# Kernel optimization log

Measured on AMD Instinct MI355X. Metric: run time of the kernel, lower is better.

## Reference

```python
import jax, jax.numpy as jnp
import numpy as np

B, S, E, H = 4, 2048, 1024, 16
D = E // H  # head_size = 64

def setup_inputs() -> dict:
    key = jax.random.key(0)
    ks = jax.random.split(key, 10)
    s_e = E ** -0.5
    s_4e = (4 * E) ** -0.5
    inp = {
        "x": jax.random.normal(ks[0], (B, S, E), dtype=jnp.float32),
        # per-head Q/K/V weights, stacked: [H, E, D], no bias
        "Wq": jax.random.normal(ks[1], (H, E, D), dtype=jnp.float32) * s_e,
        "Wk": jax.random.normal(ks[2], (H, E, D), dtype=jnp.float32) * s_e,
        "Wv": jax.random.normal(ks[3], (H, E, D), dtype=jnp.float32) * s_e,
        "Wo": jax.random.normal(ks[4], (E, E), dtype=jnp.float32) * s_e,
        "bo": jax.random.normal(ks[5], (E,), dtype=jnp.float32) * 0.01,
        "W1": jax.random.normal(ks[6], (E, 4 * E), dtype=jnp.float32) * s_e,
        "b1": jax.random.normal(ks[7], (4 * E,), dtype=jnp.float32) * 0.01,
        "W2": jax.random.normal(ks[8], (4 * E, E), dtype=jnp.float32) * s_4e,
        "b2": jax.random.normal(ks[9], (E,), dtype=jnp.float32) * 0.01,
    }
    return inp

def reference(x, Wq, Wk, Wv, Wo, bo, W1, b1, W2, b2):
    b, s, e = x.shape
    # NOTE: original scales by embedding_size**-0.5 (Size of x), not head_size
    scale = e ** -0.5
    q = jnp.einsum("bse,hed->bhsd", x, Wq)
    k = jnp.einsum("bse,hed->bhsd", x, Wk)
    v = jnp.einsum("bse,hed->bhsd", x, Wv)
    scores = jnp.einsum("bhsd,bhtd->bhst", q, k) * scale
    causal = jnp.tril(jnp.ones((s, s), dtype=bool))
    scores = jnp.where(causal, scores, -jnp.inf)
    weights = jax.nn.softmax(scores, axis=-1)
    attn = jnp.einsum("bhst,bhtd->bhsd", weights, v)  # [B,H,S,D]
    # concat heads along last dim: [B,S,H*D]
    attn = attn.transpose(0, 2, 1, 3).reshape(b, s, e)
    y = attn @ Wo + bo
    x = x + y  # residual (no LayerNorm applied in original forward)
    h = jax.nn.relu(x @ W1 + b1)
    ffn = h @ W2 + b2
    return x + ffn
```

## Files before the change

kernel.cpp:

```cpp
#include <hip/hip_runtime.h>
#include <stdint.h>

#define B_ 4
#define S_ 2048
#define E_ 1024
#define H_ 16
#define D_ 64

typedef unsigned short u16;
typedef u16 u16x8 __attribute__((ext_vector_type(8)));
typedef __bf16 bf16x8 __attribute__((ext_vector_type(8)));
typedef float f32x4 __attribute__((ext_vector_type(4)));

__device__ __forceinline__ float bf2f(u16 x) {
  unsigned int v = ((unsigned int)x) << 16;
  return __builtin_bit_cast(float, v);
}
__device__ __forceinline__ u16 f2bf(float f) {
  unsigned int u = __builtin_bit_cast(unsigned int, f);
  unsigned int r = (u + 0x7fffu + ((u >> 16) & 1u)) >> 16;
  return (u16)r;
}

__device__ __forceinline__ void gl2lds16(const u16* g, u16* l) {
  __builtin_amdgcn_global_load_lds(
      (const __attribute__((address_space(1))) void*)g,
      (__attribute__((address_space(3))) void*)l, 16, 0, 0);
}

__global__ __launch_bounds__(256) void cast_bf16_k(const float* __restrict__ src,
                                                   u16* __restrict__ dst, long n) {
  long i = ((long)blockIdx.x * 256 + threadIdx.x) * 8;
  if (i + 8 <= n) {
    f32x4 a = *(const f32x4*)(src + i), b = *(const f32x4*)(src + i + 4);
    u16x8 o;
#pragma unroll
    for (int j = 0; j < 4; j++) { o[j] = f2bf(a[j]); o[j + 4] = f2bf(b[j]); }
    *(u16x8*)(dst + i) = o;
  }
}

__global__ __launch_bounds__(256) void castT_k(const float* __restrict__ src,
                                               u16* __restrict__ dst, int R, int C) {
  long bofs = (long)blockIdx.z * R * C;
  src += bofs; dst += bofs;
  __shared__ u16 t[32][33];
  int c0 = blockIdx.x * 32, r0 = blockIdx.y * 32;
  int lc = threadIdx.x & 31, lr8 = threadIdx.x >> 5;
#pragma unroll
  for (int i = 0; i < 4; i++) {
    int lr = lr8 + i * 8;
    t[lr][lc] = f2bf(src[(long)(r0 + lr) * C + c0 + lc]);
  }
  __syncthreads();
#pragma unroll
  for (int i = 0; i < 4; i++) {
    int lr = lr8 + i * 8;
    dst[(long)(c0 + lr) * R + r0 + lc] = t[lc][lr];
  }
}

__global__ __launch_bounds__(256) void vT_k(const u16* __restrict__ QKV,
                                            u16* __restrict__ VTg) {
  int bh = blockIdx.z, d0 = blockIdx.y * 32, t0 = blockIdx.x * 32;
  int b = bh >> 4, h = bh & 15;
  __shared__ u16 t[32][33];
  int lc = threadIdx.x & 31, lr8 = threadIdx.x >> 5;
#pragma unroll
  for (int i = 0; i < 4; i++) {
    int lr = lr8 + i * 8;
    t[lr][lc] = QKV[(long)(b * S_ + t0 + lr) * 3072 + 2048 + h * 64 + d0 + lc];
  }
  __syncthreads();
#pragma unroll
  for (int i = 0; i < 4; i++) {
    int lr = lr8 + i * 8;
    VTg[((long)bh * 64 + d0 + lr) * S_ + t0 + lc] = t[lc][lr];
  }
}

template <bool AF32, bool CF32>
__global__ __launch_bounds__(256) void gemm128(const void* __restrict__ Av,
                                               const u16* __restrict__ BT,
                                               void* __restrict__ Cv,
                                               const float* __restrict__ bias,
                                               const float* __restrict__ resid,
                                               int M, int N, int K, int relu,
                                               u16* __restrict__ Cbf) {
  __shared__ u16 As[128 * 32];
  __shared__ u16 Bs[128 * 32];
  const int tid = threadIdx.x;
  const int wave = tid >> 6, lane = tid & 63;
  const int m0 = blockIdx.y * 128, n0 = blockIdx.x * 128;
  const int wm = wave >> 1, wn = wave & 1;
  const int fr = lane & 15, quad = lane >> 4;

  f32x4 acc[4][4] = {};

  const int srow = wave * 32 + (lane >> 2);
  const int skcol = (lane & 3) * 8;

  for (int k0 = 0; k0 < K; k0 += 32) {
    __syncthreads();
    if (AF32) {
      const float* Ap = (const float*)Av + (long)(m0 + (tid >> 1)) * K + k0 + (tid & 1) * 16;
      f32x4 f0 = *(const f32x4*)Ap, f1 = *(const f32x4*)(Ap + 4);
      f32x4 f2 = *(const f32x4*)(Ap + 8), f3 = *(const f32x4*)(Ap + 12);
      u16x8 p0, p1;
#pragma unroll
      for (int j = 0; j < 4; j++) {
        p0[j] = f2bf(f0[j]); p0[j + 4] = f2bf(f1[j]);
        p1[j] = f2bf(f2[j]); p1[j + 4] = f2bf(f3[j]);
      }
      *(u16x8*)&As[(tid >> 1) * 32 + (tid & 1) * 16] = p0;
      *(u16x8*)&As[(tid >> 1) * 32 + (tid & 1) * 16 + 8] = p1;
    } else {
      const u16* Ag = (const u16*)Av + (long)(m0 + srow) * K + k0 + skcol;
      gl2lds16(Ag, &As[(wave * 32) * 32]);
      gl2lds16(Ag + 16 * (long)K, &As[(wave * 32 + 16) * 32]);
    }
    {
      const u16* Bg = BT + (long)(n0 + srow) * K + k0 + skcol;
      gl2lds16(Bg, &Bs[(wave * 32) * 32]);
      gl2lds16(Bg + 16 * (long)K, &Bs[(wave * 32 + 16) * 32]);
    }
    __syncthreads();

    bf16x8 af[4], bfr[4];
#pragma unroll
    for (int mi = 0; mi < 4; mi++)
      af[mi] = __builtin_bit_cast(bf16x8, *(const u16x8*)&As[(wm * 64 + mi * 16 + fr) * 32 + quad * 8]);
#pragma unroll
    for (int ni = 0; ni < 4; ni++)
      bfr[ni] = __builtin_bit_cast(bf16x8, *(const u16x8*)&Bs[(wn * 64 + ni * 16 + fr) * 32 + quad * 8]);
#pragma unroll
    for (int mi = 0; mi < 4; mi++)
#pragma unroll
      for (int ni = 0; ni < 4; ni++)
        acc[mi][ni] = __builtin_amdgcn_mfma_f32_16x16x32_bf16(af[mi], bfr[ni], acc[mi][ni], 0, 0, 0);
  }

#pragma unroll
  for (int mi = 0; mi < 4; mi++)
#pragma unroll
    for (int ni = 0; ni < 4; ni++)
#pragma unroll
      for (int r = 0; r < 4; r++) {
        int gm = m0 + wm * 64 + mi * 16 + quad * 4 + r;
        int gn = n0 + wn * 64 + ni * 16 + fr;
        float v = acc[mi][ni][r];
        if (bias) v += bias[gn];
        if (resid) v += resid[(long)gm * N + gn];
        if (relu) v = fmaxf(v, 0.f);
        if (CF32) ((float*)Cv)[(long)gm * N + gn] = v;
        else      ((u16*)Cv)[(long)gm * N + gn] = f2bf(v);
        if (Cbf) Cbf[(long)gm * N + gn] = f2bf(v);
      }
}

__device__ __forceinline__ bf16x8 ldfrag32(const u16* base, int r, int quad) {
  int u = (r * 32 + quad * 8) ^ (((r >> 3) & 1) << 4);
  return __builtin_bit_cast(bf16x8, *(const u16x8*)(base + u));
}

template <bool CF32>
__global__ __launch_bounds__(512) void gemm2ph(const u16* __restrict__ A,
                                               const u16* __restrict__ BT,
                                               void* __restrict__ Cv,
                                               const float* __restrict__ bias,
                                               const float* __restrict__ resid,
                                               int M, int N, int K, int relu,
                                               u16* __restrict__ Cbf) {
  (void)M;
  constexpr int BM = 256, BN = 128, BK = 32;
  constexpr int AU = BM * BK;
  constexpr int BU = BN * BK;
  constexpr int BUF = AU + BU;

  __shared__ u16 sm[2 * BUF];
  const int tid = threadIdx.x;
  const int wave = tid >> 6, lane = tid & 63;
  const int wm = wave >> 1, wn = wave & 1;
  const int fr = lane & 15, quad = lane >> 4;

  const int nbx = gridDim.x;
  const int nwg = nbx * (int)gridDim.y;
  const int wgid = blockIdx.y * nbx + blockIdx.x;
  const int qq = nwg >> 3, rr = nwg & 7;
  const int xcd = wgid & 7, loc = wgid >> 3;
  const int sw = (xcd < rr ? xcd * (qq + 1) : rr * (qq + 1) + (xcd - rr) * qq) + loc;
  const int n0 = (sw % nbx) * BN;
  const int m0 = (sw / nbx) * BM;

  const int NT = K / BK;

  f32x4 acc[4][4] = {};

  const int sc_ = (tid & 3) * 8;
  const int sr_ = tid >> 2;
  const int wbase = wave << 9;

  const int rA = wm * 64 + fr;
  const int rB = wn * 64 + fr;

  {
    u16* buf = sm;
#pragma unroll
    for (int h = 0; h < 2; h++) {
      int r = h * 128 + sr_;
      int c = sc_ ^ (((r >> 3) & 1) << 4);
      gl2lds16(A + (size_t)(m0 + r) * K + c, buf + h * 4096 + wbase);
    }
    {
      int c = sc_ ^ (((sr_ >> 3) & 1) << 4);
      gl2lds16(BT + (size_t)(n0 + sr_) * K + c, buf + AU + wbase);
    }
  }
  asm volatile("s_waitcnt vmcnt(0)" ::: "memory");
  __builtin_amdgcn_s_barrier();

  for (int t = 0; t < NT; ++t) {
    u16* cb = sm + (t & 1) * BUF;
    u16* nb = sm + ((t + 1) & 1) * BUF;

    if (t + 1 < NT) {
      const int k0 = (t + 1) * BK;
#pragma unroll
      for (int h = 0; h < 2; h++) {
        int r = h * 128 + sr_;
        int c = sc_ ^ (((r >> 3) & 1) << 4);
        gl2lds16(A + (size_t)(m0 + r) * K + k0 + c, nb + h * 4096 + wbase);
      }
      {
        int c = sc_ ^ (((sr_ >> 3) & 1) << 4);
        gl2lds16(BT + (size_t)(n0 + sr_) * K + k0 + c, nb + AU + wbase);
      }
    }

    bf16x8 aF[4], bF[4];
#pragma unroll
    for (int mi = 0; mi < 4; ++mi) aF[mi] = ldfrag32(cb, rA + mi * 16, quad);
#pragma unroll
    for (int ni = 0; ni < 4; ++ni) bF[ni] = ldfrag32(cb + AU, rB + ni * 16, quad);

    asm volatile("s_waitcnt lgkmcnt(0)" ::: "memory");
    __builtin_amdgcn_sched_barrier(0);
    __builtin_amdgcn_s_setprio(1);
#pragma unroll
    for (int mi = 0; mi < 4; ++mi)
#pragma unroll
      for (int ni = 0; ni < 4; ++ni)
        acc[mi][ni] = __builtin_amdgcn_mfma_f32_16x16x32_bf16(aF[mi], bF[ni], acc[mi][ni], 0, 0, 0);
    __builtin_amdgcn_s_setprio(0);

    asm volatile("s_waitcnt vmcnt(0)" ::: "memory");
    __builtin_amdgcn_s_barrier();
  }

#pragma unroll
  for (int mi = 0; mi < 4; ++mi)
#pragma unroll
    for (int ni = 0; ni < 4; ++ni)
#pragma unroll
      for (int r = 0; r < 4; ++r) {
        int gm = m0 + wm * 64 + mi * 16 + quad * 4 + r;
        int gn = n0 + wn * 64 + ni * 16 + fr;
        float v = acc[mi][ni][r];
        if (bias) v += bias[gn];
        if (resid) v += resid[(long)gm * N + gn];
        if (relu) v = fmaxf(v, 0.f);
        if (CF32) ((float*)Cv)[(long)gm * N + gn] = v;
        else      ((u16*)Cv)[(long)gm * N + gn] = f2bf(v);
        if (Cbf) Cbf[(long)gm * N + gn] = f2bf(v);
      }
}

__global__ __launch_bounds__(256) void attn_mfma3(const u16* __restrict__ QKV,
                                                  const u16* __restrict__ VTg,
                                                  u16* __restrict__ attn) {
  int p = blockIdx.x, h = blockIdx.y, b = blockIdx.z;
  int tid = threadIdx.x;
  int wq = tid >> 6, lane = tid & 63;
  int fr = lane & 15, quad = lane >> 4;
  int kf = quad * 8;

  __shared__ u16 Qs[64][72];
  __shared__ u16 Ks[64][72];
  __shared__ u16 Vt[64][72];
  __shared__ u16 Ps[4][16][72];

  const u16* base = QKV + (long)b * S_ * 3072;
  const u16* vbase = VTg + (long)(b * 16 + h) * 64 * S_;
  int st = tid >> 2;
  int sd = (tid & 3) * 16;

  for (int ti = 0; ti < 2; ti++) {
    int qt = ti ? (31 - p) : p;

    {
      const u16* qr = base + (long)(qt * 64 + st) * 3072 + h * 64 + sd;
      u16x8 a = *(const u16x8*)qr, d = *(const u16x8*)(qr + 8);
      u16x8 oa, od;
#pragma unroll
      for (int j = 0; j < 8; j++) {
        oa[j] = f2bf(bf2f(a[j]) * 0.03125f);
        od[j] = f2bf(bf2f(d[j]) * 0.03125f);
      }
      *(u16x8*)&Qs[st][sd] = oa;
      *(u16x8*)&Qs[st][sd + 8] = od;
    }
    __syncthreads();
    bf16x8 qf0 = __builtin_bit_cast(bf16x8, *(const u16x8*)&Qs[wq * 16 + fr][kf]);
    bf16x8 qf1 = __builtin_bit_cast(bf16x8, *(const u16x8*)&Qs[wq * 16 + fr][32 + kf]);

    f32x4 acc[4] = {};
    float l[4] = {0.f, 0.f, 0.f, 0.f};

    for (int c = 0; c <= qt; c++) {
      int t0 = c * 64;
      __syncthreads();
      {
        const u16* kr = base + (long)(t0 + st) * 3072 + 1024 + h * 64 + sd;
        u16x8 k0 = *(const u16x8*)kr, k1 = *(const u16x8*)(kr + 8);
        const u16* vr = vbase + (long)st * S_ + t0 + sd;
        u16x8 v0 = *(const u16x8*)vr, v1 = *(const u16x8*)(vr + 8);
        *(u16x8*)&Ks[st][sd] = k0;
        *(u16x8*)&Ks[st][sd + 8] = k1;
        *(u16x8*)&Vt[st][sd] = v0;
        *(u16x8*)&Vt[st][sd + 8] = v1;
      }
      __syncthreads();

      f32x4 sc[4] = {};
#pragma unroll
      for (int nt = 0; nt < 4; nt++) {
        bf16x8 b0 = __builtin_bit_cast(bf16x8, *(const u16x8*)&Ks[nt * 16 + fr][kf]);
        bf16x8 b1 = __builtin_bit_cast(bf16x8, *(const u16x8*)&Ks[nt * 16 + fr][32 + kf]);
        sc[nt] = __builtin_amdgcn_mfma_f32_16x16x32_bf16(qf0, b0, sc[nt], 0, 0, 0);
        sc[nt] = __builtin_amdgcn_mfma_f32_16x16x32_bf16(qf1, b1, sc[nt], 0, 0, 0);
      }

      if (c == qt) {
        int qloc = wq * 16 + quad * 4;
#pragma unroll
        for (int nt = 0; nt < 4; nt++)
#pragma unroll
          for (int r = 0; r < 4; r++)
            if (nt * 16 + fr > qloc + r) sc[nt][r] = -1e30f;
      }

#pragma unroll
      for (int nt = 0; nt < 4; nt++)
#pragma unroll
        for (int r = 0; r < 4; r++) {
          float pv = __expf(sc[nt][r]);
          sc[nt][r] = pv;
          l[r] += pv;
        }

#pragma unroll
      for (int nt = 0; nt < 4; nt++)
#pragma unroll
        for (int r = 0; r < 4; r++)
          Ps[wq][quad * 4 + r][nt * 16 + fr] = f2bf(sc[nt][r]);

      bf16x8 pa0 = __builtin_bit_cast(bf16x8, *(const u16x8*)&Ps[wq][fr][kf]);
      bf16x8 pa1 = __builtin_bit_cast(bf16x8, *(const u16x8*)&Ps[wq][fr][32 + kf]);
#pragma unroll
      for (int nt = 0; nt < 4; nt++) {
        bf16x8 vb0 = __builtin_bit_cast(bf16x8, *(const u16x8*)&Vt[nt * 16 + fr][kf]);
        bf16x8 vb1 = __builtin_bit_cast(bf16x8, *(const u16x8*)&Vt[nt * 16 + fr][32 + kf]);
        acc[nt] = __builtin_amdgcn_mfma_f32_16x16x32_bf16(pa0, vb0, acc[nt], 0, 0, 0);
        acc[nt] = __builtin_amdgcn_mfma_f32_16x16x32_bf16(pa1, vb1, acc[nt], 0, 0, 0);
      }
    }

#pragma unroll
    for (int r = 0; r < 4; r++)
#pragma unroll
      for (int off = 1; off < 16; off <<= 1) l[r] += __shfl_xor(l[r], off);

    long row = (long)b * S_ + qt * 64 + wq * 16 + quad * 4;
#pragma unroll
    for (int nt = 0; nt < 4; nt++)
#pragma unroll
      for (int r = 0; r < 4; r++)
        attn[(row + r) * 1024 + h * 64 + nt * 16 + fr] = f2bf(acc[nt][r] / l[r]);
  }
}

extern "C" void kernel_launch(void* const* d_in, const int* in_sizes, int n_in,
                              void* d_out, int out_size, void* d_ws, size_t ws_size,
                              hipStream_t stream) {
  (void)in_sizes; (void)n_in; (void)out_size;
  const float* x  = (const float*)d_in[0];
  const float* Wq = (const float*)d_in[1];
  const float* Wk = (const float*)d_in[2];
  const float* Wv = (const float*)d_in[3];
  const float* Wo = (const float*)d_in[4];
  const float* bo = (const float*)d_in[5];
  const float* W1 = (const float*)d_in[6];
  const float* b1 = (const float*)d_in[7];
  const float* W2 = (const float*)d_in[8];
  const float* b2 = (const float*)d_in[9];
  float* out = (float*)d_out;

  char* ws = (char*)d_ws;
  u16*   QKV  = (u16*)(ws);
  u16*   attn = (u16*)(ws + 50331648);
  u16*   hbuf = (u16*)(ws);
  float* x1   = (float*)(ws + 67108864);
  u16*   VTg  = (u16*)(ws + 67108864);
  u16*   xb   = (u16*)(ws + 83886080);
  u16*   WT   = (u16*)(ws + 100663296);
  u16*   WoT  = (u16*)(ws + 106954752);
  u16*   W1T  = (u16*)(ws + 109051904);
  u16*   W2T  = (u16*)(ws + 117440512);
  u16*   x1b  = (u16*)(ws + 125829120);
  bool bigws = ws_size >= (size_t)142606336;

  cast_bf16_k<<<4096, 256, 0, stream>>>(x, xb, (long)8192 * 1024);
  castT_k<<<dim3(2, 32, 16), 256, 0, stream>>>(Wq, WT, 1024, 64);
  castT_k<<<dim3(2, 32, 16), 256, 0, stream>>>(Wk, WT + 1048576, 1024, 64);
  castT_k<<<dim3(2, 32, 16), 256, 0, stream>>>(Wv, WT + 2097152, 1024, 64);
  castT_k<<<dim3(32, 32, 1), 256, 0, stream>>>(Wo, WoT, 1024, 1024);
  castT_k<<<dim3(128, 32, 1), 256, 0, stream>>>(W1, W1T, 1024, 4096);
  castT_k<<<dim3(32, 128, 1), 256, 0, stream>>>(W2, W2T, 4096, 1024);

  gemm2ph<false><<<dim3(24, 32), 512, 0, stream>>>(xb, WT, QKV, nullptr, nullptr, 8192, 3072, 1024, 0, nullptr);
  vT_k<<<dim3(64, 2, 64), 256, 0, stream>>>(QKV, VTg);
  attn_mfma3<<<dim3(16, H_, B_), 256, 0, stream>>>(QKV, VTg, attn);
  gemm2ph<true><<<dim3(8, 32), 512, 0, stream>>>(attn, WoT, x1, bo, x, 8192, 1024, 1024, 0, bigws ? x1b : nullptr);
  if (bigws)
    gemm2ph<false><<<dim3(32, 32), 512, 0, stream>>>(x1b, W1T, hbuf, b1, nullptr, 8192, 4096, 1024, 1, nullptr);
  else
    gemm128<true, false><<<dim3(32, 64), 256, 0, stream>>>(x1, W1T, hbuf, b1, nullptr, 8192, 4096, 1024, 1, nullptr);
  gemm2ph<true><<<dim3(8, 32), 512, 0, stream>>>(hbuf, W2T, out, b2, x1, 8192, 1024, 4096, 0, nullptr);
}
```

Baseline: 561.1 us.

## Triple-buffer LDS in GEMM kernel to prefetch two K-tiles ahead

Replaces the double-buffered GEMM main loop with a three-stage LDS ring that issues global-to-LDS loads two K iterations ahead. Each wait uses vmcnt(3) so only the older tile's loads must finish, which lets one tile's loads stay in flight across the MFMA block. The aim is to hide global memory latency behind compute in all four GEMMs. In exchange, LDS use rises from 48KB to 72KB per block, which could lower occupancy.

```diff
diff --git a/kernel.cpp b/kernel.cpp
--- a/kernel.cpp
+++ b/kernel.cpp
@@ -163,21 +163,35 @@
   return __builtin_bit_cast(bf16x8, *(const u16x8*)(base + u));
 }
 
+__device__ __forceinline__ void stage_tile(const u16* __restrict__ A,
+                                           const u16* __restrict__ BT, int K,
+                                           int m0, int n0, int k0,
+                                           u16* __restrict__ buf,
+                                           int sr_, int sc_, int wbase) {
+#pragma unroll
+  for (int h = 0; h < 2; h++) {
+    int r = h * 128 + sr_;
+    int c = sc_ ^ (((r >> 3) & 1) << 4);
+    gl2lds16(A + (size_t)(m0 + r) * K + k0 + c, buf + h * 4096 + wbase);
+  }
+  int c = sc_ ^ (((sr_ >> 3) & 1) << 4);
+  gl2lds16(BT + (size_t)(n0 + sr_) * K + k0 + c, buf + 8192 + wbase);
+}
+
 template <bool CF32>
-__global__ __launch_bounds__(512) void gemm2ph(const u16* __restrict__ A,
-                                               const u16* __restrict__ BT,
-                                               void* __restrict__ Cv,
-                                               const float* __restrict__ bias,
-                                               const float* __restrict__ resid,
-                                               int M, int N, int K, int relu,
-                                               u16* __restrict__ Cbf) {
+__global__ __launch_bounds__(512) void gemm3b(const u16* __restrict__ A,
+                                              const u16* __restrict__ BT,
+                                              void* __restrict__ Cv,
+                                              const float* __restrict__ bias,
+                                              const float* __restrict__ resid,
+                                              int M, int N, int K, int relu,
+                                              u16* __restrict__ Cbf) {
   (void)M;
   constexpr int BM = 256, BN = 128, BK = 32;
   constexpr int AU = BM * BK;
-  constexpr int BU = BN * BK;
-  constexpr int BUF = AU + BU;
-
-  __shared__ u16 sm[2 * BUF];
+  constexpr int BUF = AU + BN * BK;
+
+  __shared__ u16 sm[3 * BUF];
   const int tid = threadIdx.x;
   const int wave = tid >> 6, lane = tid & 63;
   const int wm = wave >> 1, wn = wave & 1;
@@ -203,38 +217,22 @@
   const int rA = wm * 64 + fr;
   const int rB = wn * 64 + fr;
 
-  {
-    u16* buf = sm;
-#pragma unroll
-    for (int h = 0; h < 2; h++) {
-      int r = h * 128 + sr_;
-      int c = sc_ ^ (((r >> 3) & 1) << 4);
-      gl2lds16(A + (size_t)(m0 + r) * K + c, buf + h * 4096 + wbase);
-    }
-    {
-      int c = sc_ ^ (((sr_ >> 3) & 1) << 4);
-      gl2lds16(BT + (size_t)(n0 + sr_) * K + c, buf + AU + wbase);
-    }
-  }
-  asm volatile("s_waitcnt vmcnt(0)" ::: "memory");
+  stage_tile(A, BT, K, m0, n0, 0, sm, sr_, sc_, wbase);
+  if (NT > 1) {
+    stage_tile(A, BT, K, m0, n0, BK, sm + BUF, sr_, sc_, wbase);
+    asm volatile("s_waitcnt vmcnt(3)" ::: "memory");
+  } else {
+    asm volatile("s_waitcnt vmcnt(0)" ::: "memory");
+  }
   __builtin_amdgcn_s_barrier();
 
+  int cur = 0;
   for (int t = 0; t < NT; ++t) {
-    u16* cb = sm + (t & 1) * BUF;
-    u16* nb = sm + ((t + 1) & 1) * BUF;
-
-    if (t + 1 < NT) {
-      const int k0 = (t + 1) * BK;
-#pragma unroll
-      for (int h = 0; h < 2; h++) {
-        int r = h * 128 + sr_;
-        int c = sc_ ^ (((r >> 3) & 1) << 4);
-        gl2lds16(A + (size_t)(m0 + r) * K + k0 + c, nb + h * 4096 + wbase);
-      }
-      {
-        int c = sc_ ^ (((sr_ >> 3) & 1) << 4);
-        gl2lds16(BT + (size_t)(n0 + sr_) * K + k0 + c, nb + AU + wbase);
-      }
+    u16* cb = sm + cur * BUF;
+
+    if (t + 2 < NT) {
+      int s2 = cur + 2; if (s2 >= 3) s2 -= 3;
+      stage_tile(A, BT, K, m0, n0, (t + 2) * BK, sm + s2 * BUF, sr_, sc_, wbase);
     }
 
     bf16x8 aF[4], bF[4];
@@ -253,8 +251,10 @@
         acc[mi][ni] = __builtin_amdgcn_mfma_f32_16x16x32_bf16(aF[mi], bF[ni], acc[mi][ni], 0, 0, 0);
     __builtin_amdgcn_s_setprio(0);
 
-    asm volatile("s_waitcnt vmcnt(0)" ::: "memory");
+    if (t + 2 < NT) asm volatile("s_waitcnt vmcnt(3)" ::: "memory");
+    else            asm volatile("s_waitcnt vmcnt(0)" ::: "memory");
     __builtin_amdgcn_s_barrier();
+    cur = cur + 1; if (cur >= 3) cur -= 3;
   }
 
 #pragma unroll
@@ -427,13 +427,13 @@
   castT_k<<<dim3(128, 32, 1), 256, 0, stream>>>(W1, W1T, 1024, 4096);
   castT_k<<<dim3(32, 128, 1), 256, 0, stream>>>(W2, W2T, 4096, 1024);
 
-  gemm2ph<false><<<dim3(24, 32), 512, 0, stream>>>(xb, WT, QKV, nullptr, nullptr, 8192, 3072, 1024, 0, nullptr);
+  gemm3b<false><<<dim3(24, 32), 512, 0, stream>>>(xb, WT, QKV, nullptr, nullptr, 8192, 3072, 1024, 0, nullptr);
   vT_k<<<dim3(64, 2, 64), 256, 0, stream>>>(QKV, VTg);
   attn_mfma3<<<dim3(16, H_, B_), 256, 0, stream>>>(QKV, VTg, attn);
-  gemm2ph<true><<<dim3(8, 32), 512, 0, stream>>>(attn, WoT, x1, bo, x, 8192, 1024, 1024, 0, bigws ? x1b : nullptr);
+  gemm3b<true><<<dim3(8, 32), 512, 0, stream>>>(attn, WoT, x1, bo, x, 8192, 1024, 1024, 0, bigws ? x1b : nullptr);
   if (bigws)
-    gemm2ph<false><<<dim3(32, 32), 512, 0, stream>>>(x1b, W1T, hbuf, b1, nullptr, 8192, 4096, 1024, 1, nullptr);
+    gemm3b<false><<<dim3(32, 32), 512, 0, stream>>>(x1b, W1T, hbuf, b1, nullptr, 8192, 4096, 1024, 1, nullptr);
   else
     gemm128<true, false><<<dim3(32, 64), 256, 0, stream>>>(x1, W1T, hbuf, b1, nullptr, 8192, 4096, 1024, 1, nullptr);
-  gemm2ph<true><<<dim3(8, 32), 512, 0, stream>>>(hbuf, W2T, out, b2, x1, 8192, 1024, 4096, 0, nullptr);
-}
+  gemm3b<true><<<dim3(8, 32), 512, 0, stream>>>(hbuf, W2T, out, b2, x1, 8192, 1024, 4096, 0, nullptr);
+}
```

Result: faster. 534.4 us (median of 3 runs) (-4.8%).
